# Kernel optimization log

Hardware: AMD Instinct MI355X
Metric: run time of the kernel (lower is better)

Reference implementation:

```python
import jax, jax.numpy as jnp
import numpy as np

N_GOAL, N_OBS, N_TASK = 16384, 65536, 8192
E1, E2 = 1048576, 1048576
B = 256            # graphs in batch
F, S = 128, 64     # dim_features, dim_state


def setup_inputs() -> dict:
    key = jax.random.key(0)
    ks = jax.random.split(key, 16)
    inp = {
        "x_goal": jax.random.normal(ks[0], (N_GOAL, F), jnp.float32),
        "x_obs": jax.random.normal(ks[1], (N_OBS, F), jnp.float32),
        "x_task": jax.random.normal(ks[2], (N_TASK, S), jnp.float32),
        "ei_go_src": jax.random.randint(ks[3], (E1,), 0, N_GOAL),
        "ei_go_dst": jax.random.randint(ks[4], (E1,), 0, N_OBS),
        "ei_ot_src": jax.random.randint(ks[5], (E2,), 0, N_OBS),
        "ei_ot_dst": jax.random.randint(ks[6], (E2,), 0, N_TASK),
        # contiguous graph assignment: 32 task nodes per graph
        "task_batch": jnp.arange(N_TASK) // (N_TASK // B),
        # GinStandardMLP (state_gin): Lin(F,S)-ReLU-Lin(S,S)-ReLU
        "W1": jax.random.normal(ks[7], (F, S), jnp.float32) * 0.05,
        "b1": jnp.zeros((S,), jnp.float32),
        "W2": jax.random.normal(ks[8], (S, S), jnp.float32) * 0.05,
        "b2": jnp.zeros((S,), jnp.float32),
        # GinUnactivatedMLP (action_gin): Lin(S,S)-ReLU-Lin(S,1)
        "W3": jax.random.normal(ks[9], (S, S), jnp.float32) * 0.05,
        "b3": jnp.zeros((S,), jnp.float32),
        "W4": jax.random.normal(ks[10], (S, 1), jnp.float32) * 0.05,
        "b4": jnp.zeros((1,), jnp.float32),
        # critic head: Lin(2,8)-ReLU-Lin(8,1)
        "Wc1": jax.random.normal(ks[11], (2, 8), jnp.float32) * 0.5,
        "bc1": jnp.zeros((8,), jnp.float32),
        "Wc2": jax.random.normal(ks[12], (8, 1), jnp.float32) * 0.5,
        "bc2": jnp.zeros((1,), jnp.float32),
    }
    return inp


def reference(x_goal, x_obs, x_task,
              ei_go_src, ei_go_dst, ei_ot_src, ei_ot_dst, task_batch,
              W1, b1, W2, b2, W3, b3, W4, b4, Wc1, bc1, Wc2, bc2):
    # --- state_gin: GINConv((goal, obs)), eps=0 ---
    agg1 = jax.ops.segment_sum(x_goal[ei_go_src], ei_go_dst, num_segments=N_OBS)
    h = x_obs + agg1                              # (1+eps)*x_dst + sum_j x_src
    h = jax.nn.relu(h @ W1 + b1)
    x1 = jax.nn.relu(h @ W2 + b2)                 # [N_OBS, S]

    # --- action_gin: GINConv((obs, task)), eps=0 ---
    agg2 = jax.ops.segment_sum(x1[ei_ot_src], ei_ot_dst, num_segments=N_TASK)
    g = x_task + agg2
    g = jax.nn.relu(g @ W3 + b3)
    x2 = g @ W4 + b4                              # [N_TASK, 1]

    # --- critic path: global max / mean pool over task nodes per graph ---
    max_pool = jax.ops.segment_max(x2, task_batch, num_segments=B)   # [B, 1]
    cnt = jax.ops.segment_sum(jnp.ones((N_TASK, 1), x2.dtype), task_batch, num_segments=B)
    mean_pool = jax.ops.segment_sum(x2, task_batch, num_segments=B) / cnt  # [B, 1]

    pooled = jnp.concatenate([max_pool.max(axis=1, keepdims=True),
                              mean_pool.mean(axis=1, keepdims=True)], axis=1)  # [B, 2]
    out = jax.nn.relu(pooled @ Wc1 + bc1) @ Wc2 + bc2                 # [B, 1]
    return out.squeeze(-1)                                            # [B]
```

## Files before the change

### kernel.cpp

```cpp
#include <hip/hip_runtime.h>
#include <hip/hip_bf16.h>


#define NB 512
#define BUCKET_CAP 2816

__global__ __launch_bounds__(256) void gemm_k128(
    const float* __restrict__ X, const float* __restrict__ W,
    float* __restrict__ out, int M)
{
    __shared__ float Ws[128 * 64];
    __shared__ float Xs[16 * 132];
    const int tid = threadIdx.x;
    for (int i = tid; i < 128 * 64 / 4; i += 256)
        ((float4*)Ws)[i] = ((const float4*)W)[i];
    const int row0 = blockIdx.x * 16;
    for (int i = tid; i < 16 * 32; i += 256) {
        int r = i >> 5, c4 = i & 31;
        float4 v = ((const float4*)(X + (size_t)(row0 + r) * 128))[c4];
        *((float4*)(Xs + r * 132 + c4 * 4)) = v;
    }
    __syncthreads();
    const int rl = tid >> 4;
    const int cg = (tid & 15) * 4;
    float a0 = 0.f, a1 = 0.f, a2 = 0.f, a3 = 0.f;
    const float* xr = Xs + rl * 132;
    #pragma unroll 8
    for (int k = 0; k < 128; ++k) {
        float xv = xr[k];
        float4 wv = *((const float4*)(Ws + k * 64 + cg));
        a0 = fmaf(xv, wv.x, a0);
        a1 = fmaf(xv, wv.y, a1);
        a2 = fmaf(xv, wv.z, a2);
        a3 = fmaf(xv, wv.w, a3);
    }
    float4 o; o.x = a0; o.y = a1; o.z = a2; o.w = a3;
    *((float4*)(out + (size_t)(row0 + rl) * 64 + cg)) = o;
}

template <int BSH>
__global__ __launch_bounds__(256) void bin_edges(
    const int* __restrict__ src, const int* __restrict__ dst,
    int* __restrict__ gcur, int* __restrict__ pairs)
{
    constexpr int ROWM = (1 << BSH) - 1;
    __shared__ int hist[NB];
    __shared__ int cur[NB];
    const int tid = threadIdx.x;
    for (int i = tid; i < NB; i += 256) hist[i] = 0;
    __syncthreads();
    const int base = blockIdx.x * 4096;
    const int4* d4 = (const int4*)(dst + base);
    const int4* s4 = (const int4*)(src + base);
    int4 dv[4];
    #pragma unroll
    for (int k = 0; k < 4; ++k) {
        dv[k] = d4[k * 256 + tid];
        atomicAdd(&hist[dv[k].x >> BSH], 1);
        atomicAdd(&hist[dv[k].y >> BSH], 1);
        atomicAdd(&hist[dv[k].z >> BSH], 1);
        atomicAdd(&hist[dv[k].w >> BSH], 1);
    }
    __syncthreads();
    for (int i = tid; i < NB; i += 256)
        cur[i] = atomicAdd(&gcur[i], hist[i]);
    __syncthreads();
    #pragma unroll
    for (int k = 0; k < 4; ++k) {
        int4 sv = s4[k * 256 + tid];
        int d, s, b, p;
        d = dv[k].x; s = sv.x; b = d >> BSH; p = atomicAdd(&cur[b], 1);
        if (p < BUCKET_CAP) pairs[(size_t)b * BUCKET_CAP + p] = ((d & ROWM) << 17) | s;
        d = dv[k].y; s = sv.y; b = d >> BSH; p = atomicAdd(&cur[b], 1);
        if (p < BUCKET_CAP) pairs[(size_t)b * BUCKET_CAP + p] = ((d & ROWM) << 17) | s;
        d = dv[k].z; s = sv.z; b = d >> BSH; p = atomicAdd(&cur[b], 1);
        if (p < BUCKET_CAP) pairs[(size_t)b * BUCKET_CAP + p] = ((d & ROWM) << 17) | s;
        d = dv[k].w; s = sv.w; b = d >> BSH; p = atomicAdd(&cur[b], 1);
        if (p < BUCKET_CAP) pairs[(size_t)b * BUCKET_CAP + p] = ((d & ROWM) << 17) | s;
    }
}

__global__ __launch_bounds__(1024) void gather_mlp_obs(
    const int* __restrict__ pairs, const int* __restrict__ cnt,
    const float* __restrict__ xg1, const float* __restrict__ obs,
    const float* __restrict__ b1, const float* __restrict__ W2,
    const float* __restrict__ b2, float* __restrict__ x1)
{
    constexpr int ROWS = 128;
    __shared__ int ssrc[BUCKET_CAP];
    __shared__ int offs[ROWS + 1];
    __shared__ int cur[ROWS];
    __shared__ int sc[ROWS];
    __shared__ float W2s[64 * 64];
    __shared__ float hb[16 * 64];
    const int tid = threadIdx.x;
    const int b = blockIdx.x;

    ((float4*)W2s)[tid] = ((const float4*)W2)[tid];
    if (tid < ROWS) cur[tid] = 0;
    __syncthreads();
    int n = cnt[b];
    if (n > BUCKET_CAP) n = BUCKET_CAP;
    const int* bp = pairs + (size_t)b * BUCKET_CAP;

    for (int i = tid; i < n; i += 1024)
        atomicAdd(&cur[bp[i] >> 17], 1);
    __syncthreads();
    if (tid < ROWS) sc[tid] = cur[tid];
    __syncthreads();
    for (int off = 1; off < ROWS; off <<= 1) {
        int v = 0;
        if (tid < ROWS && tid >= off) v = sc[tid - off];
        __syncthreads();
        if (tid < ROWS) sc[tid] += v;
        __syncthreads();
    }
    if (tid < ROWS) {
        int ex = (tid == 0) ? 0 : sc[tid - 1];
        offs[tid] = ex;
        cur[tid] = ex;
        if (tid == ROWS - 1) offs[ROWS] = sc[tid];
    }
    __syncthreads();
    for (int i = tid; i < n; i += 1024) {
        int p = bp[i];
        int pos = atomicAdd(&cur[p >> 17], 1);
        ssrc[pos] = p & 0x1FFFF;
    }
    __syncthreads();
    const int wv = tid >> 6;
    const int lane = tid & 63;
    const float bb1 = b1[lane];
    const float bb2 = b2[lane];
    float* hp = hb + wv * 64;
    for (int r = wv; r < ROWS; r += 16) {
        int beg = offs[r], end = offs[r + 1];
        float a0 = 0.f, a1 = 0.f, a2 = 0.f, a3 = 0.f;
        int e = beg;
        for (; e + 4 <= end; e += 4) {
            int s0 = ssrc[e], s1 = ssrc[e + 1], s2 = ssrc[e + 2], s3 = ssrc[e + 3];
            a0 += xg1[(size_t)s0 * 64 + lane];
            a1 += xg1[(size_t)s1 * 64 + lane];
            a2 += xg1[(size_t)s2 * 64 + lane];
            a3 += xg1[(size_t)s3 * 64 + lane];
        }
        for (; e < end; ++e)
            a0 += xg1[(size_t)ssrc[e] * 64 + lane];
        size_t gi = (((size_t)b * ROWS) + r) * 64 + lane;
        float acc = (a0 + a1) + (a2 + a3) + obs[gi];
        hp[lane] = fmaxf(acc + bb1, 0.f);
        float a = bb2;
        #pragma unroll 16
        for (int k = 0; k < 64; ++k)
            a = fmaf(hp[k], W2s[k * 64 + lane], a);
        x1[gi] = fmaxf(a, 0.f);
    }
}

__global__ __launch_bounds__(1024) void gather_mlp_task(
    const int* __restrict__ pairs, const int* __restrict__ cnt,
    const float* __restrict__ x1, const float* __restrict__ x_task,
    const float* __restrict__ W3, const float* __restrict__ b3,
    const float* __restrict__ W4, const float* __restrict__ b4,
    float* __restrict__ x2)
{
    constexpr int ROWS = 16;
    __shared__ int ssrc[BUCKET_CAP];
    __shared__ int offs[ROWS + 1];
    __shared__ int cur[ROWS];
    __shared__ int sc[ROWS];
    __shared__ float W3s[64 * 64];
    __shared__ float hb[16 * 64];
    const int tid = threadIdx.x;
    const int b = blockIdx.x;

    ((float4*)W3s)[tid] = ((const float4*)W3)[tid];
    if (tid < ROWS) cur[tid] = 0;
    __syncthreads();
    int n = cnt[b];
    if (n > BUCKET_CAP) n = BUCKET_CAP;
    const int* bp = pairs + (size_t)b * BUCKET_CAP;

    for (int i = tid; i < n; i += 1024)
        atomicAdd(&cur[bp[i] >> 17], 1);
    __syncthreads();
    if (tid < ROWS) sc[tid] = cur[tid];
    __syncthreads();
    for (int off = 1; off < ROWS; off <<= 1) {
        int v = 0;
        if (tid < ROWS && tid >= off) v = sc[tid - off];
        __syncthreads();
        if (tid < ROWS) sc[tid] += v;
        __syncthreads();
    }
    if (tid < ROWS) {
        int ex = (tid == 0) ? 0 : sc[tid - 1];
        offs[tid] = ex;
        cur[tid] = ex;
        if (tid == ROWS - 1) offs[ROWS] = sc[tid];
    }
    __syncthreads();
    for (int i = tid; i < n; i += 1024) {
        int p = bp[i];
        int pos = atomicAdd(&cur[p >> 17], 1);
        ssrc[pos] = p & 0x1FFFF;
    }
    __syncthreads();

    const int wv = tid >> 6;
    const int lane = tid & 63;
    const int r = wv;
    const int row = b * ROWS + r;
    int beg = offs[r], end = offs[r + 1];
    float a0 = 0.f, a1 = 0.f, a2 = 0.f, a3 = 0.f;
    float a4 = 0.f, a5 = 0.f, a6 = 0.f, a7 = 0.f;
    int e = beg;
    for (; e + 8 <= end; e += 8) {
        int s0 = ssrc[e],     s1 = ssrc[e + 1], s2 = ssrc[e + 2], s3 = ssrc[e + 3];
        int s4 = ssrc[e + 4], s5 = ssrc[e + 5], s6 = ssrc[e + 6], s7 = ssrc[e + 7];
        a0 += x1[(size_t)s0 * 64 + lane];
        a1 += x1[(size_t)s1 * 64 + lane];
        a2 += x1[(size_t)s2 * 64 + lane];
        a3 += x1[(size_t)s3 * 64 + lane];
        a4 += x1[(size_t)s4 * 64 + lane];
        a5 += x1[(size_t)s5 * 64 + lane];
        a6 += x1[(size_t)s6 * 64 + lane];
        a7 += x1[(size_t)s7 * 64 + lane];
    }
    for (; e < end; ++e)
        a0 += x1[(size_t)ssrc[e] * 64 + lane];
    float t = ((a0 + a1) + (a2 + a3)) + ((a4 + a5) + (a6 + a7))
            + x_task[(size_t)row * 64 + lane];
    float* hp = hb + wv * 64;
    hp[lane] = t;
    float a = b3[lane];
    #pragma unroll 16
    for (int k = 0; k < 64; ++k)
        a = fmaf(hp[k], W3s[k * 64 + lane], a);
    float p = fmaxf(a, 0.f) * W4[lane];
    p += __shfl_xor(p, 1);
    p += __shfl_xor(p, 2);
    p += __shfl_xor(p, 4);
    p += __shfl_xor(p, 8);
    p += __shfl_xor(p, 16);
    p += __shfl_xor(p, 32);
    if (lane == 0)
        x2[row] = p + b4[0];
}

__global__ __launch_bounds__(256) void pool_critic(
    const float* __restrict__ x2, const float* __restrict__ Wc1,
    const float* __restrict__ bc1, const float* __restrict__ Wc2,
    const float* __restrict__ bc2, float* __restrict__ out)
{
    int b = threadIdx.x;
    const float* p = x2 + b * 32;
    float mx = -1e30f, sm = 0.f;
    #pragma unroll
    for (int i = 0; i < 32; ++i) { float v = p[i]; mx = fmaxf(mx, v); sm += v; }
    float mn = sm * (1.f / 32.f);
    float o = bc2[0];
    #pragma unroll
    for (int j = 0; j < 8; ++j) {
        float t = fmaxf(mx * Wc1[j] + mn * Wc1[8 + j] + bc1[j], 0.f);
        o = fmaf(t, Wc2[j], o);
    }
    out[b] = o;
}

extern "C" void kernel_launch(void* const* d_in, const int* in_sizes, int n_in,
                              void* d_out, int out_size, void* d_ws, size_t ws_size,
                              hipStream_t stream)
{
    const float* x_goal = (const float*)d_in[0];
    const float* x_obs  = (const float*)d_in[1];
    const float* x_task = (const float*)d_in[2];
    const int* go_src = (const int*)d_in[3];
    const int* go_dst = (const int*)d_in[4];
    const int* ot_src = (const int*)d_in[5];
    const int* ot_dst = (const int*)d_in[6];
    const float* W1  = (const float*)d_in[8];
    const float* b1  = (const float*)d_in[9];
    const float* W2  = (const float*)d_in[10];
    const float* b2  = (const float*)d_in[11];
    const float* W3  = (const float*)d_in[12];
    const float* b3  = (const float*)d_in[13];
    const float* W4  = (const float*)d_in[14];
    const float* b4  = (const float*)d_in[15];
    const float* Wc1 = (const float*)d_in[16];
    const float* bc1 = (const float*)d_in[17];
    const float* Wc2 = (const float*)d_in[18];
    const float* bc2 = (const float*)d_in[19];
    float* out = (float*)d_out;

    const int N_GOAL = 16384, N_OBS = 65536, N_TASK = 8192;
    const int E1 = in_sizes[3], E2 = in_sizes[5];

    char* w = (char*)d_ws;
    float* obs    = (float*)w;  w += (size_t)N_OBS * 64 * 4;
    float* x1     = (float*)w;  w += (size_t)N_OBS * 64 * 4;
    float* xg1    = (float*)w;  w += (size_t)N_GOAL * 64 * 4;
    float* x2     = (float*)w;  w += (size_t)N_TASK * 4;
    int*   pairs1 = (int*)w;    w += (size_t)NB * BUCKET_CAP * 4;
    int*   pairs2 = (int*)w;    w += (size_t)NB * BUCKET_CAP * 4;
    int*   gcur1  = (int*)w;    w += NB * 4;
    int*   gcur2  = (int*)w;    w += NB * 4;

    hipMemsetAsync(gcur1, 0, 2 * NB * 4, stream);

    bin_edges<7><<<E1 / 4096, 256, 0, stream>>>(go_src, go_dst, gcur1, pairs1);
    bin_edges<4><<<E2 / 4096, 256, 0, stream>>>(ot_src, ot_dst, gcur2, pairs2);
    gemm_k128<<<N_GOAL / 16, 256, 0, stream>>>(x_goal, W1, xg1, N_GOAL);
    gemm_k128<<<N_OBS / 16, 256, 0, stream>>>(x_obs, W1, obs, N_OBS);
    gather_mlp_obs<<<NB, 1024, 0, stream>>>(pairs1, gcur1, xg1, obs, b1, W2, b2, x1);
    gather_mlp_task<<<NB, 1024, 0, stream>>>(pairs2, gcur2, x1, x_task, W3, b3, W4, b4, x2);
    pool_critic<<<1, 256, 0, stream>>>(x2, Wc1, bc1, Wc2, bc2, out);
}
```

Baseline: 264.2 us.

## Merge launches, fuse pooling into task kernel, transpose weights and warp-scan offsets

Merges the two edge-binning launches into one kernel and the two first-layer GEMMs into one, which removes several launch gaps. The task-stage buckets change to one per graph (32 rows), so the per-graph max/mean pooling and critic head can run inside the same kernel, and the separate pool launch disappears. The gather kernels replace the multi-barrier shared-memory prefix scan with a single-wave shuffle scan and keep the edge words in registers instead of reading them twice from global memory. The dense 64x64 matvec now uses a transposed, padded weight tile read as float4. The cost is fewer task blocks (256 instead of 512), each doing more serial work, plus larger bucket capacity and a single thread finishing the pooling.

```diff
diff --git a/kernel.cpp b/kernel.cpp
--- a/kernel.cpp
+++ b/kernel.cpp
@@ -2,19 +2,24 @@
 #include <hip/hip_bf16.h>
 
 
-#define NB 512
-#define BUCKET_CAP 2816
-
-__global__ __launch_bounds__(256) void gemm_k128(
-    const float* __restrict__ X, const float* __restrict__ W,
-    float* __restrict__ out, int M)
+#define CAP1 2816
+#define CAP2 5120
+
+__global__ __launch_bounds__(256) void gemm_all(
+    const float* __restrict__ x_goal, const float* __restrict__ x_obs,
+    const float* __restrict__ W, float* __restrict__ xg1,
+    float* __restrict__ obs)
 {
     __shared__ float Ws[128 * 64];
     __shared__ float Xs[16 * 132];
     const int tid = threadIdx.x;
+    const float* X;
+    float* O;
+    int row0;
+    if (blockIdx.x < 1024) { X = x_goal; O = xg1; row0 = blockIdx.x * 16; }
+    else                   { X = x_obs;  O = obs; row0 = (blockIdx.x - 1024) * 16; }
     for (int i = tid; i < 128 * 64 / 4; i += 256)
         ((float4*)Ws)[i] = ((const float4*)W)[i];
-    const int row0 = blockIdx.x * 16;
     for (int i = tid; i < 16 * 32; i += 256) {
         int r = i >> 5, c4 = i & 31;
         float4 v = ((const float4*)(X + (size_t)(row0 + r) * 128))[c4];
@@ -35,48 +40,59 @@
         a3 = fmaf(xv, wv.w, a3);
     }
     float4 o; o.x = a0; o.y = a1; o.z = a2; o.w = a3;
-    *((float4*)(out + (size_t)(row0 + rl) * 64 + cg)) = o;
-}
-
-template <int BSH>
-__global__ __launch_bounds__(256) void bin_edges(
-    const int* __restrict__ src, const int* __restrict__ dst,
-    int* __restrict__ gcur, int* __restrict__ pairs)
-{
-    constexpr int ROWM = (1 << BSH) - 1;
-    __shared__ int hist[NB];
-    __shared__ int cur[NB];
+    *((float4*)(O + (size_t)(row0 + rl) * 64 + cg)) = o;
+}
+
+__global__ __launch_bounds__(256) void bin_edges_all(
+    const int* __restrict__ go_src, const int* __restrict__ go_dst,
+    const int* __restrict__ ot_src, const int* __restrict__ ot_dst,
+    int* __restrict__ gcur1, int* __restrict__ gcur2,
+    int* __restrict__ pairs1, int* __restrict__ pairs2, int nblk1)
+{
+    __shared__ int hist[512];
+    __shared__ int cur[512];
     const int tid = threadIdx.x;
-    for (int i = tid; i < NB; i += 256) hist[i] = 0;
-    __syncthreads();
-    const int base = blockIdx.x * 4096;
+    const bool s1 = (int)blockIdx.x < nblk1;
+    const int* src = s1 ? go_src : ot_src;
+    const int* dst = s1 ? go_dst : ot_dst;
+    int* gcur  = s1 ? gcur1 : gcur2;
+    int* pairs = s1 ? pairs1 : pairs2;
+    const int bsh  = s1 ? 7 : 5;
+    const int rowm = s1 ? 127 : 31;
+    const int nb   = s1 ? 512 : 256;
+    const int cap  = s1 ? CAP1 : CAP2;
+    const int blk  = s1 ? blockIdx.x : blockIdx.x - nblk1;
+
+    for (int i = tid; i < nb; i += 256) hist[i] = 0;
+    __syncthreads();
+    const int base = blk * 4096;
     const int4* d4 = (const int4*)(dst + base);
     const int4* s4 = (const int4*)(src + base);
     int4 dv[4];
     #pragma unroll
     for (int k = 0; k < 4; ++k) {
         dv[k] = d4[k * 256 + tid];
-        atomicAdd(&hist[dv[k].x >> BSH], 1);
-        atomicAdd(&hist[dv[k].y >> BSH], 1);
-        atomicAdd(&hist[dv[k].z >> BSH], 1);
-        atomicAdd(&hist[dv[k].w >> BSH], 1);
-    }
-    __syncthreads();
-    for (int i = tid; i < NB; i += 256)
+        atomicAdd(&hist[dv[k].x >> bsh], 1);
+        atomicAdd(&hist[dv[k].y >> bsh], 1);
+        atomicAdd(&hist[dv[k].z >> bsh], 1);
+        atomicAdd(&hist[dv[k].w >> bsh], 1);
+    }
+    __syncthreads();
+    for (int i = tid; i < nb; i += 256)
         cur[i] = atomicAdd(&gcur[i], hist[i]);
     __syncthreads();
     #pragma unroll
     for (int k = 0; k < 4; ++k) {
         int4 sv = s4[k * 256 + tid];
         int d, s, b, p;
-        d = dv[k].x; s = sv.x; b = d >> BSH; p = atomicAdd(&cur[b], 1);
-        if (p < BUCKET_CAP) pairs[(size_t)b * BUCKET_CAP + p] = ((d & ROWM) << 17) | s;
-        d = dv[k].y; s = sv.y; b = d >> BSH; p = atomicAdd(&cur[b], 1);
-        if (p < BUCKET_CAP) pairs[(size_t)b * BUCKET_CAP + p] = ((d & ROWM) << 17) | s;
-        d = dv[k].z; s = sv.z; b = d >> BSH; p = atomicAdd(&cur[b], 1);
-        if (p < BUCKET_CAP) pairs[(size_t)b * BUCKET_CAP + p] = ((d & ROWM) << 17) | s;
-        d = dv[k].w; s = sv.w; b = d >> BSH; p = atomicAdd(&cur[b], 1);
-        if (p < BUCKET_CAP) pairs[(size_t)b * BUCKET_CAP + p] = ((d & ROWM) << 17) | s;
+        d = dv[k].x; s = sv.x; b = d >> bsh; p = atomicAdd(&cur[b], 1);
+        if (p < cap) pairs[(size_t)b * cap + p] = ((d & rowm) << 17) | s;
+        d = dv[k].y; s = sv.y; b = d >> bsh; p = atomicAdd(&cur[b], 1);
+        if (p < cap) pairs[(size_t)b * cap + p] = ((d & rowm) << 17) | s;
+        d = dv[k].z; s = sv.z; b = d >> bsh; p = atomicAdd(&cur[b], 1);
+        if (p < cap) pairs[(size_t)b * cap + p] = ((d & rowm) << 17) | s;
+        d = dv[k].w; s = sv.w; b = d >> bsh; p = atomicAdd(&cur[b], 1);
+        if (p < cap) pairs[(size_t)b * cap + p] = ((d & rowm) << 17) | s;
     }
 }
 
@@ -87,52 +103,64 @@
     const float* __restrict__ b2, float* __restrict__ x1)
 {
     constexpr int ROWS = 128;
-    __shared__ int ssrc[BUCKET_CAP];
+    __shared__ int ssrc[CAP1];
     __shared__ int offs[ROWS + 1];
-    __shared__ int cur[ROWS];
-    __shared__ int sc[ROWS];
-    __shared__ float W2s[64 * 64];
+    __shared__ int rcnt[ROWS];
+    __shared__ float W2t[64 * 68];
     __shared__ float hb[16 * 64];
     const int tid = threadIdx.x;
     const int b = blockIdx.x;
 
-    ((float4*)W2s)[tid] = ((const float4*)W2)[tid];
-    if (tid < ROWS) cur[tid] = 0;
+    #pragma unroll
+    for (int i = tid; i < 4096; i += 1024) {
+        int k = i >> 6, c = i & 63;
+        W2t[c * 68 + k] = W2[i];
+    }
+    if (tid < ROWS) rcnt[tid] = 0;
     __syncthreads();
     int n = cnt[b];
-    if (n > BUCKET_CAP) n = BUCKET_CAP;
-    const int* bp = pairs + (size_t)b * BUCKET_CAP;
-
-    for (int i = tid; i < n; i += 1024)
-        atomicAdd(&cur[bp[i] >> 17], 1);
-    __syncthreads();
-    if (tid < ROWS) sc[tid] = cur[tid];
-    __syncthreads();
-    for (int off = 1; off < ROWS; off <<= 1) {
-        int v = 0;
-        if (tid < ROWS && tid >= off) v = sc[tid - off];
-        __syncthreads();
-        if (tid < ROWS) sc[tid] += v;
-        __syncthreads();
-    }
-    if (tid < ROWS) {
-        int ex = (tid == 0) ? 0 : sc[tid - 1];
-        offs[tid] = ex;
-        cur[tid] = ex;
-        if (tid == ROWS - 1) offs[ROWS] = sc[tid];
-    }
-    __syncthreads();
-    for (int i = tid; i < n; i += 1024) {
-        int p = bp[i];
-        int pos = atomicAdd(&cur[p >> 17], 1);
-        ssrc[pos] = p & 0x1FFFF;
-    }
+    if (n > CAP1) n = CAP1;
+    const int* bp = pairs + (size_t)b * CAP1;
+
+    int e0 = -1, e1 = -1, e2 = -1;
+    {
+        int i = tid;
+        if (i < n) {
+            e0 = bp[i]; atomicAdd(&rcnt[e0 >> 17], 1); i += 1024;
+            if (i < n) {
+                e1 = bp[i]; atomicAdd(&rcnt[e1 >> 17], 1); i += 1024;
+                if (i < n) { e2 = bp[i]; atomicAdd(&rcnt[e2 >> 17], 1); }
+            }
+        }
+    }
+    __syncthreads();
+    if (tid < 64) {
+        int v0 = rcnt[2 * tid], v1 = rcnt[2 * tid + 1];
+        int s = v0 + v1;
+        #pragma unroll
+        for (int d = 1; d < 64; d <<= 1) {
+            int t = __shfl_up(s, d);
+            if (tid >= d) s += t;
+        }
+        int ex = s - v0 - v1;
+        offs[2 * tid] = ex;
+        offs[2 * tid + 1] = ex + v0;
+        rcnt[2 * tid] = ex;
+        rcnt[2 * tid + 1] = ex + v0;
+        if (tid == 63) offs[ROWS] = s;
+    }
+    __syncthreads();
+    if (e0 >= 0) { int p = atomicAdd(&rcnt[e0 >> 17], 1); ssrc[p] = e0 & 0x1FFFF; }
+    if (e1 >= 0) { int p = atomicAdd(&rcnt[e1 >> 17], 1); ssrc[p] = e1 & 0x1FFFF; }
+    if (e2 >= 0) { int p = atomicAdd(&rcnt[e2 >> 17], 1); ssrc[p] = e2 & 0x1FFFF; }
     __syncthreads();
     const int wv = tid >> 6;
     const int lane = tid & 63;
     const float bb1 = b1[lane];
     const float bb2 = b2[lane];
     float* hp = hb + wv * 64;
+    const float4* h4 = (const float4*)hp;
+    const float4* wrow = (const float4*)(W2t + lane * 68);
     for (int r = wv; r < ROWS; r += 16) {
         int beg = offs[r], end = offs[r + 1];
         float a0 = 0.f, a1 = 0.f, a2 = 0.f, a3 = 0.f;
@@ -150,122 +178,150 @@
         float acc = (a0 + a1) + (a2 + a3) + obs[gi];
         hp[lane] = fmaxf(acc + bb1, 0.f);
         float a = bb2;
-        #pragma unroll 16
-        for (int k = 0; k < 64; ++k)
-            a = fmaf(hp[k], W2s[k * 64 + lane], a);
+        #pragma unroll 8
+        for (int kc = 0; kc < 16; ++kc) {
+            float4 hv = h4[kc];
+            float4 wv4 = wrow[kc];
+            a = fmaf(hv.x, wv4.x, a);
+            a = fmaf(hv.y, wv4.y, a);
+            a = fmaf(hv.z, wv4.z, a);
+            a = fmaf(hv.w, wv4.w, a);
+        }
         x1[gi] = fmaxf(a, 0.f);
     }
 }
 
-__global__ __launch_bounds__(1024) void gather_mlp_task(
+__global__ __launch_bounds__(1024) void gather_mlp_task_pool(
     const int* __restrict__ pairs, const int* __restrict__ cnt,
     const float* __restrict__ x1, const float* __restrict__ x_task,
     const float* __restrict__ W3, const float* __restrict__ b3,
     const float* __restrict__ W4, const float* __restrict__ b4,
-    float* __restrict__ x2)
-{
-    constexpr int ROWS = 16;
-    __shared__ int ssrc[BUCKET_CAP];
+    const float* __restrict__ Wc1, const float* __restrict__ bc1,
+    const float* __restrict__ Wc2, const float* __restrict__ bc2,
+    float* __restrict__ out)
+{
+    constexpr int ROWS = 32;
+    __shared__ int ssrc[CAP2];
     __shared__ int offs[ROWS + 1];
-    __shared__ int cur[ROWS];
-    __shared__ int sc[ROWS];
-    __shared__ float W3s[64 * 64];
+    __shared__ int rcnt[ROWS];
+    __shared__ float W3t[64 * 68];
     __shared__ float hb[16 * 64];
+    __shared__ float xrow[ROWS];
     const int tid = threadIdx.x;
     const int b = blockIdx.x;
 
-    ((float4*)W3s)[tid] = ((const float4*)W3)[tid];
-    if (tid < ROWS) cur[tid] = 0;
+    #pragma unroll
+    for (int i = tid; i < 4096; i += 1024) {
+        int k = i >> 6, c = i & 63;
+        W3t[c * 68 + k] = W3[i];
+    }
+    if (tid < ROWS) rcnt[tid] = 0;
     __syncthreads();
     int n = cnt[b];
-    if (n > BUCKET_CAP) n = BUCKET_CAP;
-    const int* bp = pairs + (size_t)b * BUCKET_CAP;
-
-    for (int i = tid; i < n; i += 1024)
-        atomicAdd(&cur[bp[i] >> 17], 1);
-    __syncthreads();
-    if (tid < ROWS) sc[tid] = cur[tid];
-    __syncthreads();
-    for (int off = 1; off < ROWS; off <<= 1) {
-        int v = 0;
-        if (tid < ROWS && tid >= off) v = sc[tid - off];
-        __syncthreads();
-        if (tid < ROWS) sc[tid] += v;
-        __syncthreads();
-    }
-    if (tid < ROWS) {
-        int ex = (tid == 0) ? 0 : sc[tid - 1];
+    if (n > CAP2) n = CAP2;
+    const int* bp = pairs + (size_t)b * CAP2;
+
+    int e0 = -1, e1 = -1, e2 = -1, e3 = -1, e4 = -1;
+    {
+        int i = tid;
+        if (i < n) { e0 = bp[i]; atomicAdd(&rcnt[e0 >> 17], 1); i += 1024;
+        if (i < n) { e1 = bp[i]; atomicAdd(&rcnt[e1 >> 17], 1); i += 1024;
+        if (i < n) { e2 = bp[i]; atomicAdd(&rcnt[e2 >> 17], 1); i += 1024;
+        if (i < n) { e3 = bp[i]; atomicAdd(&rcnt[e3 >> 17], 1); i += 1024;
+        if (i < n) { e4 = bp[i]; atomicAdd(&rcnt[e4 >> 17], 1); } } } } }
+    }
+    __syncthreads();
+    if (tid < 32) {
+        int v = rcnt[tid];
+        int s = v;
+        #pragma unroll
+        for (int d = 1; d < 32; d <<= 1) {
+            int t = __shfl_up(s, d);
+            if (tid >= d) s += t;
+        }
+        int ex = s - v;
         offs[tid] = ex;
-        cur[tid] = ex;
-        if (tid == ROWS - 1) offs[ROWS] = sc[tid];
-    }
-    __syncthreads();
-    for (int i = tid; i < n; i += 1024) {
-        int p = bp[i];
-        int pos = atomicAdd(&cur[p >> 17], 1);
-        ssrc[pos] = p & 0x1FFFF;
-    }
+        rcnt[tid] = ex;
+        if (tid == 31) offs[ROWS] = s;
+    }
+    __syncthreads();
+    if (e0 >= 0) { int p = atomicAdd(&rcnt[e0 >> 17], 1); ssrc[p] = e0 & 0x1FFFF; }
+    if (e1 >= 0) { int p = atomicAdd(&rcnt[e1 >> 17], 1); ssrc[p] = e1 & 0x1FFFF; }
+    if (e2 >= 0) { int p = atomicAdd(&rcnt[e2 >> 17], 1); ssrc[p] = e2 & 0x1FFFF; }
+    if (e3 >= 0) { int p = atomicAdd(&rcnt[e3 >> 17], 1); ssrc[p] = e3 & 0x1FFFF; }
+    if (e4 >= 0) { int p = atomicAdd(&rcnt[e4 >> 17], 1); ssrc[p] = e4 & 0x1FFFF; }
     __syncthreads();
 
     const int wv = tid >> 6;
     const int lane = tid & 63;
-    const int r = wv;
-    const int row = b * ROWS + r;
-    int beg = offs[r], end = offs[r + 1];
-    float a0 = 0.f, a1 = 0.f, a2 = 0.f, a3 = 0.f;
-    float a4 = 0.f, a5 = 0.f, a6 = 0.f, a7 = 0.f;
-    int e = beg;
-    for (; e + 8 <= end; e += 8) {
-        int s0 = ssrc[e],     s1 = ssrc[e + 1], s2 = ssrc[e + 2], s3 = ssrc[e + 3];
-        int s4 = ssrc[e + 4], s5 = ssrc[e + 5], s6 = ssrc[e + 6], s7 = ssrc[e + 7];
-        a0 += x1[(size_t)s0 * 64 + lane];
-        a1 += x1[(size_t)s1 * 64 + lane];
-        a2 += x1[(size_t)s2 * 64 + lane];
-        a3 += x1[(size_t)s3 * 64 + lane];
-        a4 += x1[(size_t)s4 * 64 + lane];
-        a5 += x1[(size_t)s5 * 64 + lane];
-        a6 += x1[(size_t)s6 * 64 + lane];
-        a7 += x1[(size_t)s7 * 64 + lane];
-    }
-    for (; e < end; ++e)
-        a0 += x1[(size_t)ssrc[e] * 64 + lane];
-    float t = ((a0 + a1) + (a2 + a3)) + ((a4 + a5) + (a6 + a7))
-            + x_task[(size_t)row * 64 + lane];
+    const float bb3 = b3[lane];
+    const float w4l = W4[lane];
+    const float b4c = b4[0];
     float* hp = hb + wv * 64;
-    hp[lane] = t;
-    float a = b3[lane];
-    #pragma unroll 16
-    for (int k = 0; k < 64; ++k)
-        a = fmaf(hp[k], W3s[k * 64 + lane], a);
-    float p = fmaxf(a, 0.f) * W4[lane];
-    p += __shfl_xor(p, 1);
-    p += __shfl_xor(p, 2);
-    p += __shfl_xor(p, 4);
-    p += __shfl_xor(p, 8);
-    p += __shfl_xor(p, 16);
-    p += __shfl_xor(p, 32);
-    if (lane == 0)
-        x2[row] = p + b4[0];
-}
-
-__global__ __launch_bounds__(256) void pool_critic(
-    const float* __restrict__ x2, const float* __restrict__ Wc1,
-    const float* __restrict__ bc1, const float* __restrict__ Wc2,
-    const float* __restrict__ bc2, float* __restrict__ out)
-{
-    int b = threadIdx.x;
-    const float* p = x2 + b * 32;
-    float mx = -1e30f, sm = 0.f;
-    #pragma unroll
-    for (int i = 0; i < 32; ++i) { float v = p[i]; mx = fmaxf(mx, v); sm += v; }
-    float mn = sm * (1.f / 32.f);
-    float o = bc2[0];
-    #pragma unroll
-    for (int j = 0; j < 8; ++j) {
-        float t = fmaxf(mx * Wc1[j] + mn * Wc1[8 + j] + bc1[j], 0.f);
-        o = fmaf(t, Wc2[j], o);
-    }
-    out[b] = o;
+    const float4* h4 = (const float4*)hp;
+    const float4* wrow = (const float4*)(W3t + lane * 68);
+    #pragma unroll
+    for (int half = 0; half < 2; ++half) {
+        const int r = wv + half * 16;
+        const int row = b * ROWS + r;
+        int beg = offs[r], end = offs[r + 1];
+        float a0 = 0.f, a1 = 0.f, a2 = 0.f, a3 = 0.f;
+        float a4 = 0.f, a5 = 0.f, a6 = 0.f, a7 = 0.f;
+        int e = beg;
+        for (; e + 8 <= end; e += 8) {
+            int s0 = ssrc[e],     s1 = ssrc[e + 1], s2 = ssrc[e + 2], s3 = ssrc[e + 3];
+            int s4 = ssrc[e + 4], s5 = ssrc[e + 5], s6 = ssrc[e + 6], s7 = ssrc[e + 7];
+            a0 += x1[(size_t)s0 * 64 + lane];
+            a1 += x1[(size_t)s1 * 64 + lane];
+            a2 += x1[(size_t)s2 * 64 + lane];
+            a3 += x1[(size_t)s3 * 64 + lane];
+            a4 += x1[(size_t)s4 * 64 + lane];
+            a5 += x1[(size_t)s5 * 64 + lane];
+            a6 += x1[(size_t)s6 * 64 + lane];
+            a7 += x1[(size_t)s7 * 64 + lane];
+        }
+        for (; e < end; ++e)
+            a0 += x1[(size_t)ssrc[e] * 64 + lane];
+        float t = ((a0 + a1) + (a2 + a3)) + ((a4 + a5) + (a6 + a7))
+                + x_task[(size_t)row * 64 + lane];
+        hp[lane] = t;
+        float a = bb3;
+        #pragma unroll 8
+        for (int kc = 0; kc < 16; ++kc) {
+            float4 hv = h4[kc];
+            float4 wv4 = wrow[kc];
+            a = fmaf(hv.x, wv4.x, a);
+            a = fmaf(hv.y, wv4.y, a);
+            a = fmaf(hv.z, wv4.z, a);
+            a = fmaf(hv.w, wv4.w, a);
+        }
+        float p = fmaxf(a, 0.f) * w4l;
+        p += __shfl_xor(p, 1);
+        p += __shfl_xor(p, 2);
+        p += __shfl_xor(p, 4);
+        p += __shfl_xor(p, 8);
+        p += __shfl_xor(p, 16);
+        p += __shfl_xor(p, 32);
+        if (lane == 0) xrow[r] = p + b4c;
+    }
+    __syncthreads();
+    if (tid == 0) {
+        float mx = -1e30f, sm = 0.f;
+        #pragma unroll
+        for (int i = 0; i < ROWS; ++i) {
+            float v = xrow[i];
+            mx = fmaxf(mx, v);
+            sm += v;
+        }
+        float mn = sm * (1.f / 32.f);
+        float o = bc2[0];
+        #pragma unroll
+        for (int j = 0; j < 8; ++j) {
+            float t = fmaxf(mx * Wc1[j] + mn * Wc1[8 + j] + bc1[j], 0.f);
+            o = fmaf(t, Wc2[j], o);
+        }
+        out[b] = o;
+    }
 }
 
 extern "C" void kernel_launch(void* const* d_in, const int* in_sizes, int n_in,
@@ -293,26 +349,27 @@
     const float* bc2 = (const float*)d_in[19];
     float* out = (float*)d_out;
 
-    const int N_GOAL = 16384, N_OBS = 65536, N_TASK = 8192;
+    const int N_GOAL = 16384, N_OBS = 65536;
     const int E1 = in_sizes[3], E2 = in_sizes[5];
+    const int NB1 = 512, NB2 = 256;
 
     char* w = (char*)d_ws;
     float* obs    = (float*)w;  w += (size_t)N_OBS * 64 * 4;
     float* x1     = (float*)w;  w += (size_t)N_OBS * 64 * 4;
     float* xg1    = (float*)w;  w += (size_t)N_GOAL * 64 * 4;
-    float* x2     = (float*)w;  w += (size_t)N_TASK * 4;
-    int*   pairs1 = (int*)w;    w += (size_t)NB * BUCKET_CAP * 4;
-    int*   pairs2 = (int*)w;    w += (size_t)NB * BUCKET_CAP * 4;
-    int*   gcur1  = (int*)w;    w += NB * 4;
-    int*   gcur2  = (int*)w;    w += NB * 4;
-
-    hipMemsetAsync(gcur1, 0, 2 * NB * 4, stream);
-
-    bin_edges<7><<<E1 / 4096, 256, 0, stream>>>(go_src, go_dst, gcur1, pairs1);
-    bin_edges<4><<<E2 / 4096, 256, 0, stream>>>(ot_src, ot_dst, gcur2, pairs2);
-    gemm_k128<<<N_GOAL / 16, 256, 0, stream>>>(x_goal, W1, xg1, N_GOAL);
-    gemm_k128<<<N_OBS / 16, 256, 0, stream>>>(x_obs, W1, obs, N_OBS);
-    gather_mlp_obs<<<NB, 1024, 0, stream>>>(pairs1, gcur1, xg1, obs, b1, W2, b2, x1);
-    gather_mlp_task<<<NB, 1024, 0, stream>>>(pairs2, gcur2, x1, x_task, W3, b3, W4, b4, x2);
-    pool_critic<<<1, 256, 0, stream>>>(x2, Wc1, bc1, Wc2, bc2, out);
-}
+    int*   pairs1 = (int*)w;    w += (size_t)NB1 * CAP1 * 4;
+    int*   pairs2 = (int*)w;    w += (size_t)NB2 * CAP2 * 4;
+    int*   gcur1  = (int*)w;    w += NB1 * 4;
+    int*   gcur2  = (int*)w;    w += NB2 * 4;
+
+    hipMemsetAsync(gcur1, 0, (NB1 + NB2) * 4, stream);
+
+    const int nblk1 = E1 / 4096;
+    bin_edges_all<<<nblk1 + E2 / 4096, 256, 0, stream>>>(
+        go_src, go_dst, ot_src, ot_dst, gcur1, gcur2, pairs1, pairs2, nblk1);
+    gemm_all<<<(N_GOAL + N_OBS) / 16, 256, 0, stream>>>(x_goal, x_obs, W1, xg1, obs);
+    gather_mlp_obs<<<NB1, 1024, 0, stream>>>(pairs1, gcur1, xg1, obs, b1, W2, b2, x1);
+    gather_mlp_task_pool<<<NB2, 1024, 0, stream>>>(pairs2, gcur2, x1, x_task,
+                                                   W3, b3, W4, b4,
+                                                   Wc1, bc1, Wc2, bc2, out);
+}
```

After: 242.6 us. -8.2%, faster.
